# Kernel tuning notes

Measured on AMD Instinct MI355X. Metric: run time of the kernel, lower is better.

Reference implementation:

```python
import jax, jax.numpy as jnp
import numpy as np

N = 8192
D_IN = 128
D_OUT = 128


def setup_inputs() -> dict:
    key = jax.random.key(0)
    k1, k2, k3, k4 = jax.random.split(key, 4)
    x = jax.random.normal(k1, (N, D_IN), dtype=jnp.float32)
    adj = jax.random.uniform(k2, (N, N), dtype=jnp.float32)
    # nn.Linear params: weight [out, in], bias [out]
    bound = 1.0 / np.sqrt(D_IN)
    W = jax.random.uniform(k3, (D_OUT, D_IN), minval=-bound, maxval=bound, dtype=jnp.float32)
    b = jax.random.uniform(k4, (D_OUT,), minval=-bound, maxval=bound, dtype=jnp.float32)
    return {"x": x, "adj": adj, "W": W, "b": b}


def reference(x, adj, W, b):
    # Symmetric normalization: D^{-1/2} A D^{-1/2}, expressed as fused
    # row/col scaling instead of materializing diagonal matrices.
    rowsum = adj.sum(axis=1)                      # [N]
    d_inv_sqrt = jnp.power(rowsum, -0.5)
    d_inv_sqrt = jnp.where(jnp.isinf(d_inv_sqrt), 0.0, d_inv_sqrt)
    adj_norm = d_inv_sqrt[:, None] * adj * d_inv_sqrt[None, :]  # [N, N]
    h = adj_norm @ x                              # [N, D_IN]
    return h @ W.T + b                            # [N, D_OUT]
```

## Files before the change

kernel.cpp:

```cpp
#include <hip/hip_runtime.h>
#include <hip/hip_bf16.h>

typedef short bf16x8 __attribute__((ext_vector_type(8)));
typedef float f32x16 __attribute__((ext_vector_type(16)));
typedef float f32x4v __attribute__((ext_vector_type(4)));

#define GN 8192
#define GD 128
#define KSPLIT 8


__global__ __launch_bounds__(256) void k_rowcvt(const float* __restrict__ adj,
                                                float* __restrict__ s,
                                                __hip_bfloat16* __restrict__ adjb) {
  const int row = blockIdx.x;
  const int t = threadIdx.x;
  const f32x4v* p = (const f32x4v*)(adj + (size_t)row * GN);
  f32x4v v[8];
  float acc = 0.f;
#pragma unroll
  for (int i = 0; i < 8; ++i) {
    v[i] = __builtin_nontemporal_load(p + t + i * 256);
    acc += (v[i].x + v[i].y) + (v[i].z + v[i].w);
  }
#pragma unroll
  for (int off = 32; off > 0; off >>= 1) acc += __shfl_down(acc, off, 64);
  __shared__ float red[4];
  __shared__ float sbc;
  if ((t & 63) == 0) red[t >> 6] = acc;
  __syncthreads();
  if (t == 0) {
    float tot = (red[0] + red[1]) + (red[2] + red[3]);
    float sc = (tot > 0.f) ? rsqrtf(tot) : 0.f;
    sbc = sc;
    s[row] = sc;
  }
  __syncthreads();
  const float sc = sbc;
  __hip_bfloat16* orow = adjb + (size_t)row * GN;
#pragma unroll
  for (int i = 0; i < 8; ++i) {
    __hip_bfloat16 hb[4];
    hb[0] = __float2bfloat16(v[i].x * sc);
    hb[1] = __float2bfloat16(v[i].y * sc);
    hb[2] = __float2bfloat16(v[i].z * sc);
    hb[3] = __float2bfloat16(v[i].w * sc);
    *(uint2*)(orow + (size_t)(t + i * 256) * 4) = *(uint2*)hb;
  }
}

__global__ __launch_bounds__(256) void k_pack(const float* __restrict__ x,
                                              const float* __restrict__ s,
                                              __hip_bfloat16* __restrict__ xsp) {
  const int kb = blockIdx.x;
  const int t = threadIdx.x;
  __shared__ float tile[64][129];
  __shared__ float sv[64];
  if (t < 64) sv[t] = s[kb * 64 + t];
  __syncthreads();
  const float4* xp = (const float4*)(x + (size_t)kb * 64 * GD);
#pragma unroll
  for (int j = 0; j < 8; ++j) {
    int i = t + j * 256;
    int r = i >> 5, c4 = i & 31;
    float4 v = xp[i];
    float sc = sv[r];
    tile[r][c4 * 4 + 0] = v.x * sc;
    tile[r][c4 * 4 + 1] = v.y * sc;
    tile[r][c4 * 4 + 2] = v.z * sc;
    tile[r][c4 * 4 + 3] = v.w * sc;
  }
  __syncthreads();
  const int c = t >> 1, h = t & 1;
  __hip_bfloat16 buf[32];
#pragma unroll
  for (int kk = 0; kk < 32; ++kk) buf[kk] = __float2bfloat16(tile[h * 32 + kk][c]);
  __hip_bfloat16* op = xsp + (size_t)kb * (128 * 72) + c * 72 + h * 32;
#pragma unroll
  for (int j = 0; j < 4; ++j) ((uint4*)op)[j] = ((uint4*)buf)[j];
}

__global__ __launch_bounds__(256, 2) void k_gemm(const __hip_bfloat16* __restrict__ adjb,
                                                 const __hip_bfloat16* __restrict__ xsp,
                                                 float* __restrict__ part) {
  __shared__ __align__(16) __hip_bfloat16 Asm[128 * 72];
  __shared__ __align__(16) __hip_bfloat16 Bsm[128 * 72];
  const int mb = blockIdx.x;
  const int ks = blockIdx.y;
  const int t = threadIdx.x;
  const int lane = t & 63;
  const int wave = t >> 6;
  const int wm = wave >> 1, wn = wave & 1;

  f32x16 acc00, acc01, acc10, acc11;
#pragma unroll
  for (int i = 0; i < 16; ++i) {
    acc00[i] = 0.f; acc01[i] = 0.f; acc10[i] = 0.f; acc11[i] = 0.f;
  }

  const int ar = t >> 1;
  const int ah = (t & 1) * 32;
  const __hip_bfloat16* arow = adjb + (size_t)(mb * 128 + ar) * GN + ks * 1024 + ah;
  const char* bsrc_base = (const char*)(xsp + (size_t)(ks * 16) * (128 * 72));

  const int a_lds_off = ar * 72 + ah;
  const int afrag_row = wm * 64 + (lane & 31);
  const int koff = (lane >> 5) * 8;
  const int bcol0 = wn * 64 + (lane & 31);

  for (int kt = 0; kt < 16; ++kt) {
    {
      const char* bg = bsrc_base + (size_t)kt * 18432;
#pragma unroll
      for (int c = 0; c < 5; ++c) {
        int chunk = wave + c * 4;
        if (chunk < 18) {
          __builtin_amdgcn_global_load_lds(
              (const __attribute__((address_space(1))) unsigned int*)(bg + chunk * 1024 + lane * 16),
              (__attribute__((address_space(3))) unsigned int*)((char*)Bsm + chunk * 1024),
              16, 0, 0);
        }
      }
    }
    {
      const uint4* s4 = (const uint4*)(arow + (size_t)kt * 64);
      uint4 q0 = s4[0], q1 = s4[1], q2 = s4[2], q3 = s4[3];
      uint4* d = (uint4*)(Asm + a_lds_off);
      d[0] = q0; d[1] = q1; d[2] = q2; d[3] = q3;
    }
    __syncthreads();
#pragma unroll
    for (int kk = 0; kk < 64; kk += 16) {
      bf16x8 a0 = *(const bf16x8*)(Asm + afrag_row * 72 + kk + koff);
      bf16x8 a1 = *(const bf16x8*)(Asm + (afrag_row + 32) * 72 + kk + koff);
      bf16x8 b0 = *(const bf16x8*)(Bsm + bcol0 * 72 + kk + koff);
      bf16x8 b1 = *(const bf16x8*)(Bsm + (bcol0 + 32) * 72 + kk + koff);
      acc00 = __builtin_amdgcn_mfma_f32_32x32x16_bf16(a0, b0, acc00, 0, 0, 0);
      acc01 = __builtin_amdgcn_mfma_f32_32x32x16_bf16(a0, b1, acc01, 0, 0, 0);
      acc10 = __builtin_amdgcn_mfma_f32_32x32x16_bf16(a1, b0, acc10, 0, 0, 0);
      acc11 = __builtin_amdgcn_mfma_f32_32x32x16_bf16(a1, b1, acc11, 0, 0, 0);
    }
    __syncthreads();
  }

  float* pb = part + (size_t)ks * GN * GD + (size_t)(mb * 128) * GD;
#pragma unroll
  for (int reg = 0; reg < 16; ++reg) {
    int r0 = wm * 64 + (reg & 3) + 8 * (reg >> 2) + 4 * (lane >> 5);
    int c0 = wn * 64 + (lane & 31);
    pb[(size_t)r0 * GD + c0] = acc00[reg];
    pb[(size_t)r0 * GD + c0 + 32] = acc01[reg];
    pb[(size_t)(r0 + 32) * GD + c0] = acc10[reg];
    pb[(size_t)(r0 + 32) * GD + c0 + 32] = acc11[reg];
  }
}

__global__ __launch_bounds__(256) void k_out(const float* __restrict__ part,
                                             const float* __restrict__ W,
                                             const float* __restrict__ b,
                                             float* __restrict__ out) {
  __shared__ __align__(16) __hip_bfloat16 Hs[32 * 136];
  __shared__ __align__(16) __hip_bfloat16 Ws[128 * 136];
  __shared__ float bs[128];
  const int t = threadIdx.x;
  const int rowbase = blockIdx.x * 32;
  if (t < 128) bs[t] = b[t];
#pragma unroll
  for (int j = 0; j < 4; ++j) {
    int i = t + j * 256;
    int r = i >> 5, c4 = i & 31;
    size_t idx = (size_t)(rowbase + r) * GD + c4 * 4;
    float4 a = {0.f, 0.f, 0.f, 0.f};
#pragma unroll
    for (int ksl = 0; ksl < KSPLIT; ++ksl) {
      float4 p = *(const float4*)(part + idx + (size_t)ksl * GN * GD);
      a.x += p.x; a.y += p.y; a.z += p.z; a.w += p.w;
    }
    __hip_bfloat16 hb[4];
    hb[0] = __float2bfloat16(a.x);
    hb[1] = __float2bfloat16(a.y);
    hb[2] = __float2bfloat16(a.z);
    hb[3] = __float2bfloat16(a.w);
    *(uint2*)(Hs + r * 136 + c4 * 4) = *(uint2*)hb;
  }
#pragma unroll
  for (int j = 0; j < 16; ++j) {
    int i = t + j * 256;
    int o = i >> 5, k4 = i & 31;
    float4 w = *(const float4*)(W + (size_t)o * GD + k4 * 4);
    __hip_bfloat16 hb[4];
    hb[0] = __float2bfloat16(w.x);
    hb[1] = __float2bfloat16(w.y);
    hb[2] = __float2bfloat16(w.z);
    hb[3] = __float2bfloat16(w.w);
    *(uint2*)(Ws + o * 136 + k4 * 4) = *(uint2*)hb;
  }
  __syncthreads();
  const int lane = t & 63;
  const int wave = t >> 6;
  const int arow = lane & 31;
  const int koff = (lane >> 5) * 8;
  const int bcol = wave * 32 + (lane & 31);
  f32x16 acc;
#pragma unroll
  for (int i = 0; i < 16; ++i) acc[i] = 0.f;
#pragma unroll
  for (int kk = 0; kk < 128; kk += 16) {
    bf16x8 af = *(const bf16x8*)(Hs + arow * 136 + kk + koff);
    bf16x8 bf = *(const bf16x8*)(Ws + bcol * 136 + kk + koff);
    acc = __builtin_amdgcn_mfma_f32_32x32x16_bf16(af, bf, acc, 0, 0, 0);
  }
#pragma unroll
  for (int reg = 0; reg < 16; ++reg) {
    int r = (reg & 3) + 8 * (reg >> 2) + 4 * (lane >> 5);
    out[(size_t)(rowbase + r) * GD + bcol] = acc[reg] + bs[bcol];
  }
}

extern "C" void kernel_launch(void* const* d_in, const int* in_sizes, int n_in,
                              void* d_out, int out_size, void* d_ws, size_t ws_size,
                              hipStream_t stream) {
  const float* x   = (const float*)d_in[0];
  const float* adj = (const float*)d_in[1];
  const float* W   = (const float*)d_in[2];
  const float* b   = (const float*)d_in[3];
  float* out = (float*)d_out;

  float* s = (float*)d_ws;
  __hip_bfloat16* xsp  = (__hip_bfloat16*)((char*)d_ws + 32768);
  __hip_bfloat16* adjb = (__hip_bfloat16*)((char*)d_ws + 2392064);
  float* part = (float*)((char*)d_ws + 136609792);

  k_rowcvt<<<8192, 256, 0, stream>>>(adj, s, adjb);
  k_pack<<<128, 256, 0, stream>>>(x, s, xsp);
  k_gemm<<<dim3(64, KSPLIT), 256, 0, stream>>>(adjb, xsp, part);
  k_out<<<256, 256, 0, stream>>>(part, W, b, out);
}
```

Measured before the change: 398.3 us.

## Reassociate to adj·(x·Wᵀ) and reduce split-K with atomics into output

Reorders the computation so x (scaled by column norms) is multiplied by Wᵀ first, in the packing kernel, producing a bf16 Y operand for the big GEMM. The split-K partial buffers and the final reduction-plus-linear kernel are removed: the output is pre-filled with the bias and the split-K GEMM blocks atomically add their tiles into it. This avoids writing and re-reading eight fp32 partial matrices, at the cost of float atomics, which make the summation order nondeterministic, and an extra bf16 rounding of the intermediate product.

```diff
diff --git a/kernel.cpp b/kernel.cpp
--- a/kernel.cpp
+++ b/kernel.cpp
@@ -49,13 +49,16 @@
   }
 }
 
-__global__ __launch_bounds__(256) void k_pack(const float* __restrict__ x,
-                                              const float* __restrict__ s,
-                                              __hip_bfloat16* __restrict__ xsp) {
+__global__ __launch_bounds__(256) void k_packy(const float* __restrict__ x,
+                                               const float* __restrict__ s,
+                                               const float* __restrict__ W,
+                                               __hip_bfloat16* __restrict__ yp) {
+  __shared__ __align__(16) __hip_bfloat16 Xs[64 * 136];
+  __shared__ __align__(16) __hip_bfloat16 Ws[128 * 136];
+  __shared__ __align__(16) __hip_bfloat16 Yp[128 * 72];
+  __shared__ float sv[64];
   const int kb = blockIdx.x;
   const int t = threadIdx.x;
-  __shared__ float tile[64][129];
-  __shared__ float sv[64];
   if (t < 64) sv[t] = s[kb * 64 + t];
   __syncthreads();
   const float4* xp = (const float4*)(x + (size_t)kb * 64 * GD);
@@ -65,24 +68,74 @@
     int r = i >> 5, c4 = i & 31;
     float4 v = xp[i];
     float sc = sv[r];
-    tile[r][c4 * 4 + 0] = v.x * sc;
-    tile[r][c4 * 4 + 1] = v.y * sc;
-    tile[r][c4 * 4 + 2] = v.z * sc;
-    tile[r][c4 * 4 + 3] = v.w * sc;
-  }
-  __syncthreads();
-  const int c = t >> 1, h = t & 1;
-  __hip_bfloat16 buf[32];
-#pragma unroll
-  for (int kk = 0; kk < 32; ++kk) buf[kk] = __float2bfloat16(tile[h * 32 + kk][c]);
-  __hip_bfloat16* op = xsp + (size_t)kb * (128 * 72) + c * 72 + h * 32;
-#pragma unroll
-  for (int j = 0; j < 4; ++j) ((uint4*)op)[j] = ((uint4*)buf)[j];
+    __hip_bfloat16 hb[4];
+    hb[0] = __float2bfloat16(v.x * sc);
+    hb[1] = __float2bfloat16(v.y * sc);
+    hb[2] = __float2bfloat16(v.z * sc);
+    hb[3] = __float2bfloat16(v.w * sc);
+    *(uint2*)(Xs + r * 136 + c4 * 4) = *(uint2*)hb;
+  }
+#pragma unroll
+  for (int j = 0; j < 16; ++j) {
+    int i = t + j * 256;
+    int o = i >> 5, k4 = i & 31;
+    float4 w = *(const float4*)(W + (size_t)o * GD + k4 * 4);
+    __hip_bfloat16 hb[4];
+    hb[0] = __float2bfloat16(w.x);
+    hb[1] = __float2bfloat16(w.y);
+    hb[2] = __float2bfloat16(w.z);
+    hb[3] = __float2bfloat16(w.w);
+    *(uint2*)(Ws + o * 136 + k4 * 4) = *(uint2*)hb;
+  }
+  __syncthreads();
+  const int lane = t & 63;
+  const int wave = t >> 6;
+  const int mtile = wave & 1;
+  const int n0 = (wave >> 1) * 2;
+  const int koff = (lane >> 5) * 8;
+  const int arow = mtile * 32 + (lane & 31);
+  f32x16 acc0, acc1;
+#pragma unroll
+  for (int i = 0; i < 16; ++i) { acc0[i] = 0.f; acc1[i] = 0.f; }
+#pragma unroll
+  for (int kk = 0; kk < 128; kk += 16) {
+    bf16x8 af = *(const bf16x8*)(Xs + arow * 136 + kk + koff);
+    bf16x8 b0 = *(const bf16x8*)(Ws + (n0 * 32 + (lane & 31)) * 136 + kk + koff);
+    bf16x8 b1 = *(const bf16x8*)(Ws + ((n0 + 1) * 32 + (lane & 31)) * 136 + kk + koff);
+    acc0 = __builtin_amdgcn_mfma_f32_32x32x16_bf16(af, b0, acc0, 0, 0, 0);
+    acc1 = __builtin_amdgcn_mfma_f32_32x32x16_bf16(af, b1, acc1, 0, 0, 0);
+  }
+#pragma unroll
+  for (int reg = 0; reg < 16; ++reg) {
+    int kkl = mtile * 32 + (reg & 3) + 8 * (reg >> 2) + 4 * (lane >> 5);
+    int c0 = n0 * 32 + (lane & 31);
+    Yp[c0 * 72 + kkl] = __float2bfloat16(acc0[reg]);
+    Yp[(c0 + 32) * 72 + kkl] = __float2bfloat16(acc1[reg]);
+  }
+  __syncthreads();
+  const uint4* srcv = (const uint4*)Yp;
+  uint4* dstv = (uint4*)((char*)yp + (size_t)kb * 18432);
+  for (int i = t; i < 1152; i += 256) dstv[i] = srcv[i];
+}
+
+__global__ __launch_bounds__(256) void k_bias(const float* __restrict__ b,
+                                              float* __restrict__ out) {
+  __shared__ float4 bs4[32];
+  const int t = threadIdx.x;
+  if (t < 32) bs4[t] = ((const float4*)b)[t];
+  __syncthreads();
+  const int row0 = blockIdx.x * 32;
+#pragma unroll
+  for (int j = 0; j < 4; ++j) {
+    int i = t + j * 256;
+    int r = i >> 5, c4 = i & 31;
+    ((float4*)(out + (size_t)(row0 + r) * GD))[c4] = bs4[c4];
+  }
 }
 
 __global__ __launch_bounds__(256, 2) void k_gemm(const __hip_bfloat16* __restrict__ adjb,
-                                                 const __hip_bfloat16* __restrict__ xsp,
-                                                 float* __restrict__ part) {
+                                                 const __hip_bfloat16* __restrict__ yp,
+                                                 float* __restrict__ out) {
   __shared__ __align__(16) __hip_bfloat16 Asm[128 * 72];
   __shared__ __align__(16) __hip_bfloat16 Bsm[128 * 72];
   const int mb = blockIdx.x;
@@ -101,7 +154,7 @@
   const int ar = t >> 1;
   const int ah = (t & 1) * 32;
   const __hip_bfloat16* arow = adjb + (size_t)(mb * 128 + ar) * GN + ks * 1024 + ah;
-  const char* bsrc_base = (const char*)(xsp + (size_t)(ks * 16) * (128 * 72));
+  const char* bsrc_base = (const char*)yp + (size_t)(ks * 16) * 18432;
 
   const int a_lds_off = ar * 72 + ah;
   const int afrag_row = wm * 64 + (lane & 31);
@@ -143,77 +196,15 @@
     __syncthreads();
   }
 
-  float* pb = part + (size_t)ks * GN * GD + (size_t)(mb * 128) * GD;
+  float* ob = out + (size_t)(mb * 128) * GD;
 #pragma unroll
   for (int reg = 0; reg < 16; ++reg) {
     int r0 = wm * 64 + (reg & 3) + 8 * (reg >> 2) + 4 * (lane >> 5);
     int c0 = wn * 64 + (lane & 31);
-    pb[(size_t)r0 * GD + c0] = acc00[reg];
-    pb[(size_t)r0 * GD + c0 + 32] = acc01[reg];
-    pb[(size_t)(r0 + 32) * GD + c0] = acc10[reg];
-    pb[(size_t)(r0 + 32) * GD + c0 + 32] = acc11[reg];
-  }
-}
-
-__global__ __launch_bounds__(256) void k_out(const float* __restrict__ part,
-                                             const float* __restrict__ W,
-                                             const float* __restrict__ b,
-                                             float* __restrict__ out) {
-  __shared__ __align__(16) __hip_bfloat16 Hs[32 * 136];
-  __shared__ __align__(16) __hip_bfloat16 Ws[128 * 136];
-  __shared__ float bs[128];
-  const int t = threadIdx.x;
-  const int rowbase = blockIdx.x * 32;
-  if (t < 128) bs[t] = b[t];
-#pragma unroll
-  for (int j = 0; j < 4; ++j) {
-    int i = t + j * 256;
-    int r = i >> 5, c4 = i & 31;
-    size_t idx = (size_t)(rowbase + r) * GD + c4 * 4;
-    float4 a = {0.f, 0.f, 0.f, 0.f};
-#pragma unroll
-    for (int ksl = 0; ksl < KSPLIT; ++ksl) {
-      float4 p = *(const float4*)(part + idx + (size_t)ksl * GN * GD);
-      a.x += p.x; a.y += p.y; a.z += p.z; a.w += p.w;
-    }
-    __hip_bfloat16 hb[4];
-    hb[0] = __float2bfloat16(a.x);
-    hb[1] = __float2bfloat16(a.y);
-    hb[2] = __float2bfloat16(a.z);
-    hb[3] = __float2bfloat16(a.w);
-    *(uint2*)(Hs + r * 136 + c4 * 4) = *(uint2*)hb;
-  }
-#pragma unroll
-  for (int j = 0; j < 16; ++j) {
-    int i = t + j * 256;
-    int o = i >> 5, k4 = i & 31;
-    float4 w = *(const float4*)(W + (size_t)o * GD + k4 * 4);
-    __hip_bfloat16 hb[4];
-    hb[0] = __float2bfloat16(w.x);
-    hb[1] = __float2bfloat16(w.y);
-    hb[2] = __float2bfloat16(w.z);
-    hb[3] = __float2bfloat16(w.w);
-    *(uint2*)(Ws + o * 136 + k4 * 4) = *(uint2*)hb;
-  }
-  __syncthreads();
-  const int lane = t & 63;
-  const int wave = t >> 6;
-  const int arow = lane & 31;
-  const int koff = (lane >> 5) * 8;
-  const int bcol = wave * 32 + (lane & 31);
-  f32x16 acc;
-#pragma unroll
-  for (int i = 0; i < 16; ++i) acc[i] = 0.f;
-#pragma unroll
-  for (int kk = 0; kk < 128; kk += 16) {
-    bf16x8 af = *(const bf16x8*)(Hs + arow * 136 + kk + koff);
-    bf16x8 bf = *(const bf16x8*)(Ws + bcol * 136 + kk + koff);
-    acc = __builtin_amdgcn_mfma_f32_32x32x16_bf16(af, bf, acc, 0, 0, 0);
-  }
-#pragma unroll
-  for (int reg = 0; reg < 16; ++reg) {
-    int r = (reg & 3) + 8 * (reg >> 2) + 4 * (lane >> 5);
-    out[(size_t)(rowbase + r) * GD + bcol] = acc[reg] + bs[bcol];
+    atomicAdd(&ob[(size_t)r0 * GD + c0], acc00[reg]);
+    atomicAdd(&ob[(size_t)r0 * GD + c0 + 32], acc01[reg]);
+    atomicAdd(&ob[(size_t)(r0 + 32) * GD + c0], acc10[reg]);
+    atomicAdd(&ob[(size_t)(r0 + 32) * GD + c0 + 32], acc11[reg]);
   }
 }
 
@@ -227,12 +218,11 @@
   float* out = (float*)d_out;
 
   float* s = (float*)d_ws;
-  __hip_bfloat16* xsp  = (__hip_bfloat16*)((char*)d_ws + 32768);
+  __hip_bfloat16* yp   = (__hip_bfloat16*)((char*)d_ws + 32768);
   __hip_bfloat16* adjb = (__hip_bfloat16*)((char*)d_ws + 2392064);
-  float* part = (float*)((char*)d_ws + 136609792);
 
   k_rowcvt<<<8192, 256, 0, stream>>>(adj, s, adjb);
-  k_pack<<<128, 256, 0, stream>>>(x, s, xsp);
-  k_gemm<<<dim3(64, KSPLIT), 256, 0, stream>>>(adjb, xsp, part);
-  k_out<<<256, 256, 0, stream>>>(part, W, b, out);
-}
+  k_packy<<<128, 256, 0, stream>>>(x, s, W, yp);
+  k_bias<<<256, 256, 0, stream>>>(b, out);
+  k_gemm<<<dim3(64, KSPLIT), 256, 0, stream>>>(adjb, yp, out);
+}
```

Result: slower. 412.0 us (+3.4%).
